# Optimization experiments

Hardware: AMD Instinct MI355X
Metric: run time of the kernel (lower is better)

Reference implementation:

```python
import jax, jax.numpy as jnp
import numpy as np

B, N, DEG, LOOKBACK, DIM, OUT = 256, 512, 16, 5, 64, 6
E = B * N * DEG            # 2,097,152 directed edges
NN = B * N                 # 131,072 nodes
K1 = int(np.ceil(0.8 * N))    # 410 nodes kept per graph after pool1
K2 = int(np.ceil(0.8 * K1))   # 328 nodes kept per graph after pool2


def setup_inputs():
    key = jax.random.key(0)
    ks = jax.random.split(key, 14)
    x = jax.random.normal(ks[0], (NN, LOOKBACK), jnp.float32)
    # per-graph random edges, then shift into the global node index space
    local = jax.random.randint(ks[1], (2, E), 0, N)
    offsets = jnp.repeat(jnp.arange(B, dtype=jnp.int32) * N, N * DEG)
    edge_index = local + offsets[None, :]

    def lin(k, fi, fo):
        return jax.random.normal(k, (fi, fo), jnp.float32) / np.sqrt(fi)

    return {
        "x": x,
        "edge_index": edge_index,
        "c1_Wl": lin(ks[2], LOOKBACK, DIM), "c1_bl": jnp.zeros((DIM,), jnp.float32),
        "c1_Wr": lin(ks[3], LOOKBACK, DIM),
        "pool1_w": jax.random.normal(ks[4], (DIM,), jnp.float32) / np.sqrt(DIM),
        "c2_Wl": lin(ks[5], DIM, DIM), "c2_bl": jnp.zeros((DIM,), jnp.float32),
        "c2_Wr": lin(ks[6], DIM, DIM),
        "pool2_w": jax.random.normal(ks[7], (DIM,), jnp.float32) / np.sqrt(DIM),
        "lin1_W": lin(ks[8], 2 * DIM, DIM), "lin1_b": jnp.zeros((DIM,), jnp.float32),
        "lin2_W": lin(ks[9], DIM, OUT), "lin2_b": jnp.zeros((OUT,), jnp.float32),
    }


def _sage(x, src, dst, valid, Wl, bl, Wr, n_nodes):
    # PyG SAGEConv: out = lin_l(mean_{j->i} x_j) + lin_r(x_i); empty nbhd -> 0
    msg = x[src] * valid[:, None]
    s = jax.ops.segment_sum(msg, dst, num_segments=n_nodes)
    deg = jax.ops.segment_sum(valid, dst, num_segments=n_nodes)
    mean = s / jnp.maximum(deg, 1.0)[:, None]
    return mean @ Wl + bl + x @ Wr


def _topk(x, w, nb, npg, k):
    # PyG TopKPooling: score = tanh(x.w/||w||), keep top-k per graph, scale kept rows
    score = jnp.tanh((x @ w) / jnp.linalg.norm(w))
    vals, idx = jax.lax.top_k(score.reshape(nb, npg), k)     # [nb, k]
    perm = (idx + (jnp.arange(nb) * npg)[:, None]).reshape(-1)
    return x[perm] * vals.reshape(-1, 1), perm


def _readout(x, nb, k):
    r = x.reshape(nb, k, -1)
    return jnp.concatenate([r.max(axis=1), r.mean(axis=1)], axis=1)  # [gmp | gap]


def reference(x, edge_index, c1_Wl, c1_bl, c1_Wr, pool1_w,
              c2_Wl, c2_bl, c2_Wr, pool2_w, lin1_W, lin1_b, lin2_W, lin2_b):
    src, dst = edge_index[0], edge_index[1]
    valid0 = jnp.ones((E,), jnp.float32)

    h = jax.nn.relu(_sage(x, src, dst, valid0, c1_Wl, c1_bl, c1_Wr, NN))
    h, perm1 = _topk(h, pool1_w, B, N, K1)
    x1 = _readout(h, B, K1)

    # filter_adj: remap edges to pooled node ids, mask dropped edges
    n1 = B * K1
    inv = jnp.full((NN,), -1, jnp.int32).at[perm1].set(jnp.arange(n1, dtype=jnp.int32))
    s1, d1 = inv[src], inv[dst]
    valid1 = ((s1 >= 0) & (d1 >= 0)).astype(jnp.float32)
    s1 = jnp.maximum(s1, 0)
    d1 = jnp.maximum(d1, 0)

    h = jax.nn.relu(_sage(h, s1, d1, valid1, c2_Wl, c2_bl, c2_Wr, n1))
    h, _ = _topk(h, pool2_w, B, K1, K2)
    x2 = _readout(h, B, K2)

    z = x1 + x2
    z = jax.nn.relu(z @ lin1_W + lin1_b)
    return z @ lin2_W + lin2_b
```

## Files before the change

### kernel.cpp

```cpp
#include <hip/hip_runtime.h>
#include <hip/hip_bf16.h>

#define BGR   256
#define NPG1  512
#define DEG   16
#define EPG   (NPG1 * DEG)
#define LB    5
#define DIM   64
#define OUTF  6
#define NN    (BGR * NPG1)
#define EDG   (BGR * EPG)
#define K1    410
#define K2    328
#define N1    (BGR * K1)
#define K1P   (K1 + 1)
#define NR    (BGR * K1P)
#define CSRW  48
#define CSRW1 56
#define GRIDW (NR / 64)
#define GRIDA (N1 / 16)

__global__ __launch_bounds__(512)
void s1_mega_kernel(const float* __restrict__ x,
                    const int* __restrict__ eidx,
                    const float* __restrict__ Wl,
                    const float* __restrict__ bl,
                    const float* __restrict__ Wr,
                    const float* __restrict__ pw,
                    float* __restrict__ h1p,
                    float* __restrict__ x1buf,
                    unsigned short* __restrict__ csr2,
                    int* __restrict__ indeg) {
    __shared__ __align__(16) float xl[NPG1 * LB];
    __shared__ __align__(16) float ml[NPG1 * LB];
    __shared__ unsigned short lcsr1[CSRW1 * NPG1];
    __shared__ int   lcnt[NPG1];
    __shared__ __align__(16) float sc[NPG1];
    __shared__ int   rnk[NPG1];
    __shared__ __align__(16) unsigned short lcsr2[K1 * CSRW];
    __shared__ int   lcnt2[K1];
    __shared__ float redmx[8 * DIM];
    __shared__ float redsm[8 * DIM];

    const int g = blockIdx.x, t = threadIdx.x;
    const int wid = t >> 6, lane = t & 63;
    const int* __restrict__ src = eidx;
    const int* __restrict__ dst = eidx + EDG;

    {
        const float4* x4 = (const float4*)(x + (size_t)g * (NPG1 * LB));
        float4* xl4 = (float4*)xl;
        #pragma unroll
        for (int k = 0; k < 2; ++k) {
            int i = k * 512 + t;
            if (i < NPG1 * LB / 4) xl4[i] = x4[i];
        }
        lcnt[t] = 0;
        const int fill = (K1 << 16) | K1;
        int* li = (int*)lcsr2;
        for (int i = t; i < K1 * CSRW / 2; i += 512) li[i] = fill;
        if (t < DIM) h1p[((size_t)g * K1P + K1) * DIM + t] = 0.f;
    }
    __syncthreads();

    const int ebase = g * EPG;
    for (int k = 0; k < EPG / 512; ++k) {
        int e = ebase + k * 512 + t;
        int s = src[e] & (NPG1 - 1);
        int d = dst[e] & (NPG1 - 1);
        int slot = atomicAdd(&lcnt[d], 1);
        if (slot < CSRW1) lcsr1[slot * NPG1 + d] = (unsigned short)s;
    }
    __syncthreads();

    {
        const int dgf = lcnt[t];
        const int dg  = min(dgf, CSRW1);
        float s0 = 0.f, s1 = 0.f, s2 = 0.f, s3 = 0.f, s4 = 0.f;
        for (int k = 0; k < dg; ++k) {
            int s = lcsr1[k * NPG1 + t];
            const float* xp = xl + s * LB;
            s0 += xp[0]; s1 += xp[1]; s2 += xp[2]; s3 += xp[3]; s4 += xp[4];
        }
        const float invd = 1.f / fmaxf((float)dgf, 1.f);
        float m[LB]  = { s0 * invd, s1 * invd, s2 * invd, s3 * invd, s4 * invd };
        float xv[LB];
        #pragma unroll
        for (int j = 0; j < LB; ++j) { xv[j] = xl[t * LB + j]; ml[t * LB + j] = m[j]; }

        const float4* Wl4 = (const float4*)Wl;
        const float4* Wr4 = (const float4*)Wr;
        const float4* bl4 = (const float4*)bl;
        const float4* pw4 = (const float4*)pw;
        float p = 0.f, q = 0.f;
        #pragma unroll 4
        for (int d4 = 0; d4 < DIM / 4; ++d4) {
            float4 bb = bl4[d4];
            float4 ww = pw4[d4];
            float4 h = bb;
            #pragma unroll
            for (int j = 0; j < LB; ++j) {
                float4 a = Wl4[j * (DIM / 4) + d4];
                float4 b = Wr4[j * (DIM / 4) + d4];
                h.x += m[j] * a.x + xv[j] * b.x;
                h.y += m[j] * a.y + xv[j] * b.y;
                h.z += m[j] * a.z + xv[j] * b.z;
                h.w += m[j] * a.w + xv[j] * b.w;
            }
            h.x = fmaxf(h.x, 0.f); h.y = fmaxf(h.y, 0.f);
            h.z = fmaxf(h.z, 0.f); h.w = fmaxf(h.w, 0.f);
            p += h.x * ww.x + h.y * ww.y + h.z * ww.z + h.w * ww.w;
            q += ww.x * ww.x + ww.y * ww.y + ww.z * ww.z + ww.w * ww.w;
        }
        sc[t] = tanhf(p / sqrtf(q));
    }
    __syncthreads();

    {
        float my = sc[t];
        int r = 0;
        const float4* sc4 = (const float4*)sc;
        #pragma unroll 4
        for (int j4 = 0; j4 < NPG1 / 4; ++j4) {
            float4 v = sc4[j4];
            int j = 4 * j4;
            r += (v.x > my) | ((v.x == my) & (j     < t));
            r += (v.y > my) | ((v.y == my) & (j + 1 < t));
            r += (v.z > my) | ((v.z == my) & (j + 2 < t));
            r += (v.w > my) | ((v.w == my) & (j + 3 < t));
        }
        rnk[t] = r;
    }
    __syncthreads();

    {
        const int rd = rnk[t];
        if (rd < K1) {
            const int dg1 = min(lcnt[t], CSRW1);
            int vcnt = 0;
            for (int k = 0; k < dg1; ++k) {
                int s  = lcsr1[k * NPG1 + t];
                int rs = rnk[s];
                if (rs < K1) {
                    if (vcnt < CSRW) lcsr2[rd * CSRW + vcnt] = (unsigned short)rs;
                    ++vcnt;
                }
            }
            lcnt2[rd] = min(vcnt, CSRW);
        }
    }

    {
        float wlv[LB], wrv[LB];
        #pragma unroll
        for (int j = 0; j < LB; ++j) { wlv[j] = Wl[j * DIM + lane]; wrv[j] = Wr[j * DIM + lane]; }
        const float blv = bl[lane];

        float mx = -INFINITY, sm = 0.f;
        for (int n = wid; n < NPG1; n += 8) {
            int r = rnk[n];
            if (r >= K1) continue;
            const float* mp = ml + n * LB;
            const float* xp = xl + n * LB;
            float al = 0.f, ar = 0.f;
            #pragma unroll
            for (int j = 0; j < LB; ++j) {
                al += mp[j] * wlv[j];
                ar += xp[j] * wrv[j];
            }
            float acc = fmaxf(blv + al + ar, 0.f);
            float v = acc * sc[n];
            h1p[((size_t)g * K1P + r) * DIM + lane] = v;
            mx = fmaxf(mx, v);
            sm += v;
        }
        redmx[wid * DIM + lane] = mx;
        redsm[wid * DIM + lane] = sm;
    }
    __syncthreads();

    if (wid == 0) {
        float m2 = redmx[lane], s2 = redsm[lane];
        #pragma unroll
        for (int w = 1; w < 8; ++w) {
            m2 = fmaxf(m2, redmx[w * DIM + lane]);
            s2 += redsm[w * DIM + lane];
        }
        x1buf[g * 2 * DIM + lane]       = m2;
        x1buf[g * 2 * DIM + DIM + lane] = s2 * (1.0f / (float)K1);
    }

    {
        const int4* ls4 = (const int4*)lcsr2;
        int4* gs4 = (int4*)(csr2 + (size_t)g * K1 * CSRW);
        for (int i = t; i < K1 * CSRW / 8; i += 512) gs4[i] = ls4[i];
        if (t < K1) indeg[g * K1 + t] = lcnt2[t];
    }
}

__global__ __launch_bounds__(512)
void gemm2_kernel(float* __restrict__ hY,
                  float* __restrict__ Yr,
                  const float* __restrict__ Wl,
                  const float* __restrict__ bl,
                  const float* __restrict__ Wr) {
    __shared__ __align__(16) float wls[DIM * DIM];
    __shared__ __align__(16) float wrs[DIM * DIM];
    __shared__ __align__(16) float rt[64 * DIM];

    const int t = threadIdx.x, wid = t >> 6, lane = t & 63;
    const int nb = (int)blockIdx.x * 64;

    {
        const float4* W4l = (const float4*)Wl;
        const float4* W4r = (const float4*)Wr;
        const float4* R4  = (const float4*)&hY[(size_t)nb * DIM];
        float4* a = (float4*)wls;
        float4* b = (float4*)wrs;
        float4* r = (float4*)rt;
        #pragma unroll
        for (int k = 0; k < 2; ++k) {
            a[k * 512 + t] = W4l[k * 512 + t];
            b[k * 512 + t] = W4r[k * 512 + t];
            r[k * 512 + t] = R4[k * 512 + t];
        }
    }
    __syncthreads();

    const int r0 = wid * 8;
    float accl[8] = {0.f,0.f,0.f,0.f,0.f,0.f,0.f,0.f};
    float accr[8] = {0.f,0.f,0.f,0.f,0.f,0.f,0.f,0.f};
    #pragma unroll 4
    for (int j4 = 0; j4 < DIM / 4; ++j4) {
        const int jb = 4 * j4 * DIM + lane;
        float w0 = wls[jb],           w1 = wls[jb + DIM];
        float w2 = wls[jb + 2 * DIM], w3 = wls[jb + 3 * DIM];
        float u0 = wrs[jb],           u1 = wrs[jb + DIM];
        float u2 = wrs[jb + 2 * DIM], u3 = wrs[jb + 3 * DIM];
        #pragma unroll
        for (int i = 0; i < 8; ++i) {
            float4 a = *(const float4*)&rt[(r0 + i) * DIM + 4 * j4];
            accl[i] += a.x * w0 + a.y * w1 + a.z * w2 + a.w * w3;
            accr[i] += a.x * u0 + a.y * u1 + a.z * u2 + a.w * u3;
        }
    }
    const float bv = bl[lane];
    #pragma unroll
    for (int i = 0; i < 8; ++i) {
        hY[(size_t)(nb + r0 + i) * DIM + lane] = accl[i];
        Yr[(size_t)(nb + r0 + i) * DIM + lane] = accr[i] + bv;
    }
}

__global__ __launch_bounds__(256)
void gather2_kernel(const float* __restrict__ Yl,
                    float* __restrict__ Yh,
                    const unsigned short* __restrict__ csr2,
                    const int* __restrict__ indeg,
                    const float* __restrict__ pw,
                    float* __restrict__ sc2g) {
    const int t = threadIdx.x, wid = t >> 6, lane = t & 63;
    const int cid = ((int)blockIdx.x & 7) * (GRIDA / 8) + ((int)blockIdx.x >> 3);
    const int nb = __builtin_amdgcn_readfirstlane(cid * 16 + wid * 4);

    const float pwv = pw[lane];
    float q = pwv * pwv;
    #pragma unroll
    for (int o = 32; o; o >>= 1) q += __shfl_xor(q, o);
    const float inv_nrm = 1.f / sqrtf(q);

    #pragma unroll
    for (int i = 0; i < 4; ++i) {
        const int n  = nb + i;
        const int dg = indeg[n];
        const int g  = n / K1;
        const int lr = n - g * K1;
        const float* __restrict__ bp = Yl + (size_t)g * K1P * DIM;
        const int4* cr = (const int4*)(csr2 + (size_t)n * CSRW);
        float a0 = 0.f, a1 = 0.f;
        const int it = (dg + 7) >> 3;
        for (int kc = 0; kc < it; ++kc) {
            int4 wv = cr[kc];
            a0 += bp[((wv.x & 0xffff) << 6) + lane];
            a1 += bp[((wv.x >> 16)    << 6) + lane];
            a0 += bp[((wv.y & 0xffff) << 6) + lane];
            a1 += bp[((wv.y >> 16)    << 6) + lane];
            a0 += bp[((wv.z & 0xffff) << 6) + lane];
            a1 += bp[((wv.z >> 16)    << 6) + lane];
            a0 += bp[((wv.w & 0xffff) << 6) + lane];
            a1 += bp[((wv.w >> 16)    << 6) + lane];
        }
        const float invd = 1.f / fmaxf((float)dg, 1.f);
        float* yrow = Yh + (size_t)(g * K1P + lr) * DIM;
        const float h = fmaxf((a0 + a1) * invd + yrow[lane], 0.f);
        yrow[lane] = h;
        float p = h * pwv;
        #pragma unroll
        for (int o = 32; o; o >>= 1) p += __shfl_xor(p, o);
        if (lane == 0) sc2g[n] = tanhf(p * inv_nrm);
    }
}

__global__ __launch_bounds__(512)
void pool2_mlp_kernel(const float* __restrict__ sc2g,
                      const float* __restrict__ h2,
                      const float* __restrict__ x1buf,
                      const float* __restrict__ W1,
                      const float* __restrict__ b1,
                      const float* __restrict__ W2,
                      const float* __restrict__ b2,
                      float* __restrict__ out) {
    __shared__ __align__(16) float sc2[412];
    __shared__ int   rnk2[K1];
    __shared__ float redmx[8 * DIM];
    __shared__ float redsm[8 * DIM];
    __shared__ float zy[2 * DIM + DIM];

    const int g = blockIdx.x, t = threadIdx.x;
    const int wid = t >> 6, lane = t & 63;

    if (t < K1) sc2[t] = sc2g[g * K1 + t];
    if (t >= K1 && t < 412) sc2[t] = -INFINITY;
    __syncthreads();

    if (t < K1) {
        float my = sc2[t];
        int r = 0;
        const float4* sc4 = (const float4*)sc2;
        #pragma unroll 4
        for (int j4 = 0; j4 < 103; ++j4) {
            float4 v = sc4[j4];
            int j = 4 * j4;
            r += (v.x > my) | ((v.x == my) & (j     < t));
            r += (v.y > my) | ((v.y == my) & (j + 1 < t));
            r += (v.z > my) | ((v.z == my) & (j + 2 < t));
            r += (v.w > my) | ((v.w == my) & (j + 3 < t));
        }
        rnk2[t] = r;
    }
    __syncthreads();

    float mx = -INFINITY, sm = 0.f;
    for (int n = wid; n < K1; n += 8) {
        if (rnk2[n] < K2) {
            float v = h2[((size_t)g * K1P + n) * DIM + lane] * sc2[n];
            mx = fmaxf(mx, v);
            sm += v;
        }
    }
    redmx[wid * DIM + lane] = mx;
    redsm[wid * DIM + lane] = sm;
    __syncthreads();
    if (wid == 0) {
        float m2 = redmx[lane], s2 = redsm[lane];
        #pragma unroll
        for (int w = 1; w < 8; ++w) {
            m2 = fmaxf(m2, redmx[w * DIM + lane]);
            s2 += redsm[w * DIM + lane];
        }
        zy[lane]       = x1buf[g * 2 * DIM + lane]       + m2;
        zy[DIM + lane] = x1buf[g * 2 * DIM + DIM + lane] + s2 * (1.0f / (float)K2);
    }
    __syncthreads();

    if (t < DIM) {
        float a = b1[t];
        #pragma unroll 8
        for (int j = 0; j < 2 * DIM; ++j) a += zy[j] * W1[j * DIM + t];
        zy[2 * DIM + t] = fmaxf(a, 0.f);
    }
    __syncthreads();
    if (t < OUTF) {
        float a = b2[t];
        #pragma unroll
        for (int j = 0; j < DIM; ++j) a += zy[2 * DIM + j] * W2[j * OUTF + t];
        out[g * OUTF + t] = a;
    }
}

extern "C" void kernel_launch(void* const* d_in, const int* in_sizes, int n_in,
                              void* d_out, int out_size, void* d_ws, size_t ws_size,
                              hipStream_t stream) {
    (void)in_sizes; (void)n_in; (void)out_size; (void)ws_size;
    const float* x       = (const float*)d_in[0];
    const int*   eidx    = (const int*)d_in[1];
    const float* c1_Wl   = (const float*)d_in[2];
    const float* c1_bl   = (const float*)d_in[3];
    const float* c1_Wr   = (const float*)d_in[4];
    const float* pool1_w = (const float*)d_in[5];
    const float* c2_Wl   = (const float*)d_in[6];
    const float* c2_bl   = (const float*)d_in[7];
    const float* c2_Wr   = (const float*)d_in[8];
    const float* pool2_w = (const float*)d_in[9];
    const float* lin1_W  = (const float*)d_in[10];
    const float* lin1_b  = (const float*)d_in[11];
    const float* lin2_W  = (const float*)d_in[12];
    const float* lin2_b  = (const float*)d_in[13];
    float* out = (float*)d_out;

    char* w = (char*)d_ws;
    size_t off = 0;
    auto alloc = [&](size_t bytes) {
        void* p = w + off;
        off = (off + bytes + 255) & ~(size_t)255;
        return p;
    };
    float* h1p   = (float*)alloc((size_t)NR * DIM * 4);
    float* x1buf = (float*)alloc((size_t)BGR * 2 * DIM * 4);
    float* sc2g  = (float*)alloc((size_t)N1 * 4);
    int*   indeg = (int*)  alloc((size_t)N1 * 4);
    float* Yh    = (float*)alloc((size_t)NR * DIM * 4);
    unsigned short* csr2 = (unsigned short*)alloc((size_t)N1 * CSRW * 2);

    float* Yl = h1p;

    s1_mega_kernel<<<BGR, 512, 0, stream>>>(x, eidx, c1_Wl, c1_bl, c1_Wr,
                                            pool1_w, h1p, x1buf, csr2, indeg);
    gemm2_kernel<<<GRIDW, 512, 0, stream>>>(h1p, Yh, c2_Wl, c2_bl, c2_Wr);
    gather2_kernel<<<GRIDA, 256, 0, stream>>>(Yl, Yh, csr2, indeg, pool2_w, sc2g);
    pool2_mlp_kernel<<<BGR, 512, 0, stream>>>(sc2g, Yh, x1buf, lin1_W, lin1_b,
                                              lin2_W, lin2_b, out);
}
```

Before: 165.8 us.

## Double threads per graph in stage-1 kernel and split work across halves

Raises the first-stage per-graph kernel from 512 to 1024 threads. The two halves of the block split the neighbour-mean gather and the rank computation, then combine partial results through shared memory. The readout loop is spread over 16 waves instead of 8. To free shared memory, the readout reduction buffers now reuse the local CSR array and the local CSR width is trimmed from 56 to 52. This adds extra barriers, leaves half the threads idle in the dense SAGE/score step, and truncates neighbour lists for any node whose in-degree exceeds 52.

```diff
diff --git a/kernel.cpp b/kernel.cpp
--- a/kernel.cpp
+++ b/kernel.cpp
@@ -16,11 +16,11 @@
 #define K1P   (K1 + 1)
 #define NR    (BGR * K1P)
 #define CSRW  48
-#define CSRW1 56
+#define CSRW1 52
 #define GRIDW (NR / 64)
 #define GRIDA (N1 / 16)
 
-__global__ __launch_bounds__(512)
+__global__ __launch_bounds__(1024)
 void s1_mega_kernel(const float* __restrict__ x,
                     const int* __restrict__ eidx,
                     const float* __restrict__ Wl,
@@ -33,39 +33,39 @@
                     int* __restrict__ indeg) {
     __shared__ __align__(16) float xl[NPG1 * LB];
     __shared__ __align__(16) float ml[NPG1 * LB];
-    __shared__ unsigned short lcsr1[CSRW1 * NPG1];
+    __shared__ __align__(16) unsigned short lcsr1[CSRW1 * NPG1];
     __shared__ int   lcnt[NPG1];
     __shared__ __align__(16) float sc[NPG1];
     __shared__ int   rnk[NPG1];
+    __shared__ int   rhelp[NPG1];
     __shared__ __align__(16) unsigned short lcsr2[K1 * CSRW];
     __shared__ int   lcnt2[K1];
-    __shared__ float redmx[8 * DIM];
-    __shared__ float redsm[8 * DIM];
+    float* redmx = (float*)lcsr1;
+    float* redsm = redmx + 16 * DIM;
 
     const int g = blockIdx.x, t = threadIdx.x;
     const int wid = t >> 6, lane = t & 63;
+    const int n9 = t & (NPG1 - 1);
+    const int half = t >> 9;
     const int* __restrict__ src = eidx;
     const int* __restrict__ dst = eidx + EDG;
 
     {
         const float4* x4 = (const float4*)(x + (size_t)g * (NPG1 * LB));
         float4* xl4 = (float4*)xl;
-        #pragma unroll
-        for (int k = 0; k < 2; ++k) {
-            int i = k * 512 + t;
-            if (i < NPG1 * LB / 4) xl4[i] = x4[i];
-        }
-        lcnt[t] = 0;
+        if (t < NPG1 * LB / 4) xl4[t] = x4[t];
+        if (t < NPG1) lcnt[t] = 0;
         const int fill = (K1 << 16) | K1;
         int* li = (int*)lcsr2;
-        for (int i = t; i < K1 * CSRW / 2; i += 512) li[i] = fill;
+        for (int i = t; i < K1 * CSRW / 2; i += 1024) li[i] = fill;
         if (t < DIM) h1p[((size_t)g * K1P + K1) * DIM + t] = 0.f;
     }
     __syncthreads();
 
     const int ebase = g * EPG;
-    for (int k = 0; k < EPG / 512; ++k) {
-        int e = ebase + k * 512 + t;
+    #pragma unroll
+    for (int k = 0; k < EPG / 1024; ++k) {
+        int e = ebase + k * 1024 + t;
         int s = src[e] & (NPG1 - 1);
         int d = dst[e] & (NPG1 - 1);
         int slot = atomicAdd(&lcnt[d], 1);
@@ -74,72 +74,84 @@
     __syncthreads();
 
     {
-        const int dgf = lcnt[t];
+        const int dgf = lcnt[n9];
         const int dg  = min(dgf, CSRW1);
         float s0 = 0.f, s1 = 0.f, s2 = 0.f, s3 = 0.f, s4 = 0.f;
-        for (int k = 0; k < dg; ++k) {
-            int s = lcsr1[k * NPG1 + t];
+        for (int k = half; k < dg; k += 2) {
+            int s = lcsr1[k * NPG1 + n9];
             const float* xp = xl + s * LB;
             s0 += xp[0]; s1 += xp[1]; s2 += xp[2]; s3 += xp[3]; s4 += xp[4];
         }
-        const float invd = 1.f / fmaxf((float)dgf, 1.f);
-        float m[LB]  = { s0 * invd, s1 * invd, s2 * invd, s3 * invd, s4 * invd };
-        float xv[LB];
-        #pragma unroll
-        for (int j = 0; j < LB; ++j) { xv[j] = xl[t * LB + j]; ml[t * LB + j] = m[j]; }
-
-        const float4* Wl4 = (const float4*)Wl;
-        const float4* Wr4 = (const float4*)Wr;
-        const float4* bl4 = (const float4*)bl;
-        const float4* pw4 = (const float4*)pw;
-        float p = 0.f, q = 0.f;
-        #pragma unroll 4
-        for (int d4 = 0; d4 < DIM / 4; ++d4) {
-            float4 bb = bl4[d4];
-            float4 ww = pw4[d4];
-            float4 h = bb;
+        if (half == 1) {
+            float* mp = ml + n9 * LB;
+            mp[0] = s0; mp[1] = s1; mp[2] = s2; mp[3] = s3; mp[4] = s4;
+        }
+        __syncthreads();
+        if (half == 0) {
+            float* mp = ml + n9 * LB;
+            s0 += mp[0]; s1 += mp[1]; s2 += mp[2]; s3 += mp[3]; s4 += mp[4];
+            const float invd = 1.f / fmaxf((float)dgf, 1.f);
+            float m[LB]  = { s0 * invd, s1 * invd, s2 * invd, s3 * invd, s4 * invd };
+            float xv[LB];
             #pragma unroll
-            for (int j = 0; j < LB; ++j) {
-                float4 a = Wl4[j * (DIM / 4) + d4];
-                float4 b = Wr4[j * (DIM / 4) + d4];
-                h.x += m[j] * a.x + xv[j] * b.x;
-                h.y += m[j] * a.y + xv[j] * b.y;
-                h.z += m[j] * a.z + xv[j] * b.z;
-                h.w += m[j] * a.w + xv[j] * b.w;
+            for (int j = 0; j < LB; ++j) { xv[j] = xl[n9 * LB + j]; mp[j] = m[j]; }
+
+            const float4* Wl4 = (const float4*)Wl;
+            const float4* Wr4 = (const float4*)Wr;
+            const float4* bl4 = (const float4*)bl;
+            const float4* pw4 = (const float4*)pw;
+            float p = 0.f, q = 0.f;
+            #pragma unroll 4
+            for (int d4 = 0; d4 < DIM / 4; ++d4) {
+                float4 bb = bl4[d4];
+                float4 ww = pw4[d4];
+                float4 h = bb;
+                #pragma unroll
+                for (int j = 0; j < LB; ++j) {
+                    float4 a = Wl4[j * (DIM / 4) + d4];
+                    float4 b = Wr4[j * (DIM / 4) + d4];
+                    h.x += m[j] * a.x + xv[j] * b.x;
+                    h.y += m[j] * a.y + xv[j] * b.y;
+                    h.z += m[j] * a.z + xv[j] * b.z;
+                    h.w += m[j] * a.w + xv[j] * b.w;
+                }
+                h.x = fmaxf(h.x, 0.f); h.y = fmaxf(h.y, 0.f);
+                h.z = fmaxf(h.z, 0.f); h.w = fmaxf(h.w, 0.f);
+                p += h.x * ww.x + h.y * ww.y + h.z * ww.z + h.w * ww.w;
+                q += ww.x * ww.x + ww.y * ww.y + ww.z * ww.z + ww.w * ww.w;
             }
-            h.x = fmaxf(h.x, 0.f); h.y = fmaxf(h.y, 0.f);
-            h.z = fmaxf(h.z, 0.f); h.w = fmaxf(h.w, 0.f);
-            p += h.x * ww.x + h.y * ww.y + h.z * ww.z + h.w * ww.w;
-            q += ww.x * ww.x + ww.y * ww.y + ww.z * ww.z + ww.w * ww.w;
-        }
-        sc[t] = tanhf(p / sqrtf(q));
-    }
-    __syncthreads();
-
-    {
-        float my = sc[t];
+            sc[n9] = tanhf(p / sqrtf(q));
+        }
+    }
+    __syncthreads();
+
+    {
+        float my = sc[n9];
         int r = 0;
         const float4* sc4 = (const float4*)sc;
+        const int j0 = half * (NPG1 / 8);
         #pragma unroll 4
-        for (int j4 = 0; j4 < NPG1 / 4; ++j4) {
+        for (int j4 = j0; j4 < j0 + NPG1 / 8; ++j4) {
             float4 v = sc4[j4];
             int j = 4 * j4;
-            r += (v.x > my) | ((v.x == my) & (j     < t));
-            r += (v.y > my) | ((v.y == my) & (j + 1 < t));
-            r += (v.z > my) | ((v.z == my) & (j + 2 < t));
-            r += (v.w > my) | ((v.w == my) & (j + 3 < t));
-        }
-        rnk[t] = r;
-    }
-    __syncthreads();
-
-    {
-        const int rd = rnk[t];
+            r += (v.x > my) | ((v.x == my) & (j     < n9));
+            r += (v.y > my) | ((v.y == my) & (j + 1 < n9));
+            r += (v.z > my) | ((v.z == my) & (j + 2 < n9));
+            r += (v.w > my) | ((v.w == my) & (j + 3 < n9));
+        }
+        if (half == 1) rhelp[n9] = r;
+        __syncthreads();
+        if (half == 0) rnk[n9] = r + rhelp[n9];
+    }
+    __syncthreads();
+
+    if (half == 0) {
+        const int rd = rnk[n9];
         if (rd < K1) {
-            const int dg1 = min(lcnt[t], CSRW1);
+            const int dg1 = min(lcnt[n9], CSRW1);
             int vcnt = 0;
             for (int k = 0; k < dg1; ++k) {
-                int s  = lcsr1[k * NPG1 + t];
+                int s  = lcsr1[k * NPG1 + n9];
                 int rs = rnk[s];
                 if (rs < K1) {
                     if (vcnt < CSRW) lcsr2[rd * CSRW + vcnt] = (unsigned short)rs;
@@ -150,14 +162,14 @@
         }
     }
 
+    float mx = -INFINITY, sm = 0.f;
     {
         float wlv[LB], wrv[LB];
         #pragma unroll
         for (int j = 0; j < LB; ++j) { wlv[j] = Wl[j * DIM + lane]; wrv[j] = Wr[j * DIM + lane]; }
         const float blv = bl[lane];
 
-        float mx = -INFINITY, sm = 0.f;
-        for (int n = wid; n < NPG1; n += 8) {
+        for (int n = wid; n < NPG1; n += 16) {
             int r = rnk[n];
             if (r >= K1) continue;
             const float* mp = ml + n * LB;
@@ -174,15 +186,16 @@
             mx = fmaxf(mx, v);
             sm += v;
         }
-        redmx[wid * DIM + lane] = mx;
-        redsm[wid * DIM + lane] = sm;
-    }
-    __syncthreads();
-
+    }
+    __syncthreads();
+
+    redmx[wid * DIM + lane] = mx;
+    redsm[wid * DIM + lane] = sm;
+    __syncthreads();
     if (wid == 0) {
         float m2 = redmx[lane], s2 = redsm[lane];
         #pragma unroll
-        for (int w = 1; w < 8; ++w) {
+        for (int w = 1; w < 16; ++w) {
             m2 = fmaxf(m2, redmx[w * DIM + lane]);
             s2 += redsm[w * DIM + lane];
         }
@@ -193,7 +206,7 @@
     {
         const int4* ls4 = (const int4*)lcsr2;
         int4* gs4 = (int4*)(csr2 + (size_t)g * K1 * CSRW);
-        for (int i = t; i < K1 * CSRW / 8; i += 512) gs4[i] = ls4[i];
+        for (int i = t; i < K1 * CSRW / 8; i += 1024) gs4[i] = ls4[i];
         if (t < K1) indeg[g * K1 + t] = lcnt2[t];
     }
 }
@@ -414,8 +427,8 @@
 
     float* Yl = h1p;
 
-    s1_mega_kernel<<<BGR, 512, 0, stream>>>(x, eidx, c1_Wl, c1_bl, c1_Wr,
-                                            pool1_w, h1p, x1buf, csr2, indeg);
+    s1_mega_kernel<<<BGR, 1024, 0, stream>>>(x, eidx, c1_Wl, c1_bl, c1_Wr,
+                                             pool1_w, h1p, x1buf, csr2, indeg);
     gemm2_kernel<<<GRIDW, 512, 0, stream>>>(h1p, Yh, c2_Wl, c2_bl, c2_Wr);
     gather2_kernel<<<GRIDA, 256, 0, stream>>>(Yl, Yh, csr2, indeg, pool2_w, sc2g);
     pool2_mlp_kernel<<<BGR, 512, 0, stream>>>(sc2g, Yh, x1buf, lin1_W, lin1_b,
```

Result: faster. 158.6 us (-4.3%).
